# Optimization experiments

Hardware: AMD Instinct MI355X
Metric: run time of the kernel (lower is better)

## Reference

```python
import jax, jax.numpy as jnp
import numpy as np

NUM_BINS = 64  # num_bins_target == num_bins_source (defaults)
C_WIN = 1.0    # c_target == c_source (defaults)
EPS_LOG = 1e-12


def _normalise(x):
    # normalise_torch(x, 0.0, 1.0): global min-max rescale to [0, 1]
    x = x.astype(jnp.float32)
    return (x - x.min()) / (x.max() - x.min())


def _cubic_bspline(x):
    # Parzen cubic B-spline window (support |x| < 2)
    ax = jnp.abs(x)
    inner = (4.0 - 6.0 * ax * ax + 3.0 * ax * ax * ax) / 6.0
    outer = (2.0 - ax) ** 3 / 6.0
    return jnp.where(ax < 1.0, inner, jnp.where(ax < 2.0, outer, 0.0))


def setup_inputs() -> dict:
    key = jax.random.key(0)
    k1, k2 = jax.random.split(key)
    target = jax.random.uniform(k1, (2, 1, 96, 96, 96), dtype=jnp.float32)
    source = jax.random.uniform(k2, (2, 1, 96, 96, 96), dtype=jnp.float32)
    return {"target": target, "source": source}


def reference(target, source):
    # pre-processing: normalise to [0,1], flatten spatial dims -> (B, 1, N)
    t = _normalise(target).reshape(target.shape[0], target.shape[1], -1)
    s = _normalise(source).reshape(source.shape[0], source.shape[1], -1)

    # histogram bins (after normalisation max-min == 1)
    bw_t = (t.max() - t.min()) / NUM_BINS
    bw_s = (s.max() - s.min()) / NUM_BINS
    bins_t = jnp.arange(NUM_BINS, dtype=jnp.float32)[:, None] * bw_t  # (bins, 1)
    bins_s = jnp.arange(NUM_BINS, dtype=jnp.float32)[:, None] * bw_s
    eps_t = C_WIN * bw_t
    eps_s = C_WIN * bw_s

    # broadcast: (bins,1) - (B,1,N) -> (B, bins, N)
    W_t = _cubic_bspline((bins_t - t) / eps_t)
    W_s = _cubic_bspline((bins_s - s) / eps_s)

    # joint histogram: (B, bins_t, bins_s)
    hist_joint = jnp.einsum('bin,bjn->bij', W_t, W_s) / (eps_t * eps_s)

    # distributions (normalised over the WHOLE tensor, incl. batch, as in torch)
    p_joint = hist_joint / hist_joint.sum()
    p_t = p_joint.sum(axis=2)  # (B, bins_t)
    p_s = p_joint.sum(axis=1)  # (B, bins_s)

    # entropies per batch element
    H_t = -jnp.sum(p_t * jnp.log(p_t + EPS_LOG), axis=1)
    H_s = -jnp.sum(p_s * jnp.log(p_s + EPS_LOG), axis=1)
    H_j = -jnp.sum(p_joint * jnp.log(p_joint + EPS_LOG), axis=(1, 2))

    # NMI loss (nmi=True default)
    return -jnp.mean((H_t + H_s) / H_j)
```

## Files before the change

kernel.cpp:

```cpp
#include <hip/hip_runtime.h>
#include <math.h>

#define NBINS 64
#define BATCH_N 884736
#define NTOT   1769472
#define ROWB  80
#define TILE_B 5440
#define WAVE_B 10880
#define MROW 66
#define QS 190.0f
#define GBLK 216
#define GWAVES 864
#define KBLK 512

#define OFF_GHIST 256
#define OFF_KBLK 36864

typedef int  v4i __attribute__((ext_vector_type(4)));

__device__ __forceinline__ unsigned fkey(float x){
    unsigned u = __float_as_uint(x);
    return (u & 0x80000000u) ? ~u : (u | 0x80000000u);
}
__device__ __forceinline__ float fdecode(unsigned k){
    return __uint_as_float((k & 0x80000000u) ? (k ^ 0x80000000u) : ~k);
}

__device__ __forceinline__ void bw4(float u, float w[4]){
    float um = 1.f - u;
    float u2 = u*u, um2 = um*um;
    w[0] = um2*um*(1.f/6.f);
    w[3] = u2*u*(1.f/6.f);
    w[1] = 0.6666666666666667f - u2 + 0.5f*u2*u;
    w[2] = 0.6666666666666667f - um2 + 0.5f*um2*um;
}

__global__ void __launch_bounds__(256)
k_minmax(const float4* __restrict__ t4, const float4* __restrict__ s4,
         int n4, uint4* __restrict__ kblk, float* __restrict__ ghist){
    __shared__ unsigned red[4][4];

    if (blockIdx.x < 8)
        ghist[blockIdx.x*1024 + threadIdx.x] = 0.f,
        ghist[blockIdx.x*1024 + 256 + threadIdx.x] = 0.f,
        ghist[blockIdx.x*1024 + 512 + threadIdx.x] = 0.f,
        ghist[blockIdx.x*1024 + 768 + threadIdx.x] = 0.f;

    unsigned mt=0u, mnt=0u, ms=0u, mns=0u;
    int stride = gridDim.x * blockDim.x;
    for (int i = blockIdx.x*blockDim.x + threadIdx.x; i < n4; i += stride){
        float4 a = t4[i];
        float4 b = s4[i];
        mt  = max(mt,  max(max(fkey(a.x),  fkey(a.y)),  max(fkey(a.z),  fkey(a.w))));
        mnt = max(mnt, max(max(fkey(-a.x), fkey(-a.y)), max(fkey(-a.z), fkey(-a.w))));
        ms  = max(ms,  max(max(fkey(b.x),  fkey(b.y)),  max(fkey(b.z),  fkey(b.w))));
        mns = max(mns, max(max(fkey(-b.x), fkey(-b.y)), max(fkey(-b.z), fkey(-b.w))));
    }
    #pragma unroll
    for (int off = 32; off; off >>= 1){
        mt  = max(mt,  __shfl_down(mt,  off));
        mnt = max(mnt, __shfl_down(mnt, off));
        ms  = max(ms,  __shfl_down(ms,  off));
        mns = max(mns, __shfl_down(mns, off));
    }
    int wid = threadIdx.x >> 6;
    if ((threadIdx.x & 63) == 0){
        red[wid][0] = mt; red[wid][1] = mnt; red[wid][2] = ms; red[wid][3] = mns;
    }
    __syncthreads();
    if (threadIdx.x == 0){
        uint4 q;
        q.x = max(max(red[0][0], red[1][0]), max(red[2][0], red[3][0]));
        q.y = max(max(red[0][1], red[1][1]), max(red[2][1], red[3][1]));
        q.z = max(max(red[0][2], red[1][2]), max(red[2][2], red[3][2]));
        q.w = max(max(red[0][3], red[1][3]), max(red[2][3], red[3][3]));
        kblk[blockIdx.x] = q;
    }
}

__global__ void __launch_bounds__(256)
k_gemm(const float* __restrict__ t, const float* __restrict__ s,
       const uint4* __restrict__ kblk, float* __restrict__ ghist){
    __shared__ int4 smem4[2720];
    __shared__ unsigned kred[4][4];

    int tid = threadIdx.x;
    int lane = tid & 63;
    int warp = tid >> 6;
    int rrow = lane & 15;
    int kgrp = lane >> 4;
    int b = blockIdx.y;

    char* As = (char*)smem4 + warp*WAVE_B;
    char* Bs = As + TILE_B;

    {
        int4* wz = (int4*)As;
        int4 z4 = {0,0,0,0};
        #pragma unroll
        for (int i = 0; i < 11; ++i){
            int idx = i*64 + lane;
            if (idx < WAVE_B/16) wz[idx] = z4;
        }
    }

    {
        unsigned m0=0u, m1=0u, m2=0u, m3=0u;
        #pragma unroll
        for (int i = 0; i < 2; ++i){
            uint4 q = kblk[tid + i*256];
            m0 = max(m0, q.x); m1 = max(m1, q.y);
            m2 = max(m2, q.z); m3 = max(m3, q.w);
        }
        #pragma unroll
        for (int off = 32; off; off >>= 1){
            m0 = max(m0, __shfl_down(m0, off));
            m1 = max(m1, __shfl_down(m1, off));
            m2 = max(m2, __shfl_down(m2, off));
            m3 = max(m3, __shfl_down(m3, off));
        }
        if (lane == 0){
            kred[warp][0] = m0; kred[warp][1] = m1;
            kred[warp][2] = m2; kred[warp][3] = m3;
        }
        __syncthreads();
    }
    float tmax =  fdecode(max(max(kred[0][0], kred[1][0]), max(kred[2][0], kred[3][0])));
    float tmin = -fdecode(max(max(kred[0][1], kred[1][1]), max(kred[2][1], kred[3][1])));
    float smax =  fdecode(max(max(kred[0][2], kred[1][2]), max(kred[2][2], kred[3][2])));
    float smin = -fdecode(max(max(kred[0][3], kred[1][3]), max(kred[2][3], kred[3][3])));
    float tsc = 64.f / (tmax - tmin);
    float ssc = 64.f / (smax - smin);

    const float* tb = t + (size_t)b*BATCH_N;
    const float* sb = s + (size_t)b*BATCH_N;

    v4i acc[4][4];
    #pragma unroll
    for (int i = 0; i < 4; ++i)
        #pragma unroll
        for (int j = 0; j < 4; ++j)
            acc[i][j] = (v4i){0,0,0,0};

    int c0 = blockIdx.x*4 + warp;
    float tq0 = tb[(size_t)c0*64 + lane];
    float sq0 = sb[(size_t)c0*64 + lane];
    float tq1 = tb[(size_t)(c0 + GWAVES)*64 + lane];
    float sq1 = sb[(size_t)(c0 + GWAVES)*64 + lane];

    #pragma unroll 2
    for (int it = 0; it < 16; ++it){
        int cpre = c0 + (it < 14 ? (it + 2)*GWAVES : 0);
        float tnn = tb[(size_t)cpre*64 + lane];
        float snn = sb[(size_t)cpre*64 + lane];

        float vt = (tq0 - tmin) * tsc;
        float vs = (sq0 - smin) * ssc;
        int it0 = (int)floorf(vt);
        int is0 = (int)floorf(vs);
        float wt[4], wsv[4];
        bw4(vt - (float)it0, wt);
        bw4(vs - (float)is0, wsv);

        char* pa = As + it0*ROWB + lane;
        char* pb = Bs + is0*ROWB + lane;
        #pragma unroll
        for (int k = 0; k < 4; ++k){
            pa[k*ROWB] = (char)__float2int_rn(wt[k]  * QS);
            pb[k*ROWB] = (char)__float2int_rn(wsv[k] * QS);
        }

        v4i af[4], bf[4];
        #pragma unroll
        for (int m = 0; m < 4; ++m)
            af[m] = *(const v4i*)(As + (m*16 + rrow + 1)*ROWB + kgrp*16);
        #pragma unroll
        for (int n = 0; n < 4; ++n)
            bf[n] = *(const v4i*)(Bs + (n*16 + rrow + 1)*ROWB + kgrp*16);
        #pragma unroll
        for (int m = 0; m < 4; ++m)
            #pragma unroll
            for (int n = 0; n < 4; ++n)
                acc[m][n] = __builtin_amdgcn_mfma_i32_16x16x64_i8(af[m], bf[n], acc[m][n], 0, 0, 0);

        __asm__ volatile("" ::: "memory");
        #pragma unroll
        for (int k = 0; k < 4; ++k){
            pa[k*ROWB] = 0;
            pb[k*ROWB] = 0;
        }

        tq0 = tq1; sq0 = sq1;
        tq1 = tnn; sq1 = snn;
    }

    const float dq = 1.f / (QS*QS);
    float* fmw = (float*)((char*)smem4 + (warp >> 1)*(2*WAVE_B));
    __syncthreads();
    if ((warp & 1) == 0){
        #pragma unroll
        for (int m = 0; m < 4; ++m)
            #pragma unroll
            for (int n = 0; n < 4; ++n)
                #pragma unroll
                for (int r = 0; r < 4; ++r)
                    fmw[(m*16 + kgrp*4 + r)*MROW + n*16 + rrow] = (float)acc[m][n][r] * dq;
    }
    __syncthreads();
    if ((warp & 1) == 1){
        #pragma unroll
        for (int m = 0; m < 4; ++m)
            #pragma unroll
            for (int n = 0; n < 4; ++n)
                #pragma unroll
                for (int r = 0; r < 4; ++r)
                    fmw[(m*16 + kgrp*4 + r)*MROW + n*16 + rrow] += (float)acc[m][n][r] * dq;
    }
    __syncthreads();
    {
        const float* fm0 = (const float*)smem4;
        const float* fm1 = (const float*)((char*)smem4 + 2*WAVE_B);
        float* g = ghist + b*4096;
        #pragma unroll
        for (int i = 0; i < 16; ++i){
            int idx = i*256 + tid;
            int l = (idx >> 6)*MROW + (idx & 63);
            unsafeAtomicAdd(&g[idx], fm0[l] + fm1[l]);
        }
    }
}

__device__ __forceinline__ float blockReduceSum(float v, float* red){
    #pragma unroll
    for (int off = 32; off; off >>= 1) v += __shfl_down(v, off);
    int wid = threadIdx.x >> 6, lane = threadIdx.x & 63;
    __syncthreads();
    if (lane == 0) red[wid] = v;
    __syncthreads();
    return red[0] + red[1] + red[2] + red[3];
}

__global__ void k_final(const float* __restrict__ hist, float* __restrict__ out){
    __shared__ float sh[2*4096];
    __shared__ float red[4];
    int tid = threadIdx.x;
    for (int i = tid; i < 8192; i += 256) sh[i] = hist[i];
    __syncthreads();

    float loc = 0.f;
    for (int i = tid; i < 8192; i += 256) loc += sh[i];
    float total = blockReduceSum(loc, red);
    float inv = 1.f / total;

    float nmi[2];
    for (int b = 0; b < 2; ++b){
        const float* h = sh + b*4096;
        float lj = 0.f;
        for (int i = tid; i < 4096; i += 256){
            float p = h[i]*inv;
            lj += p*logf(p + 1e-12f);
        }
        float Hj = -blockReduceSum(lj, red);
        float lt = 0.f;
        if (tid < 64){
            float r = 0.f;
            for (int j = 0; j < 64; ++j) r += h[tid*64 + j];
            float p = r*inv;
            lt = p*logf(p + 1e-12f);
        }
        float Ht = -blockReduceSum(lt, red);
        float ls = 0.f;
        if (tid < 64){
            float c = 0.f;
            for (int j = 0; j < 64; ++j) c += h[j*64 + tid];
            float p = c*inv;
            ls = p*logf(p + 1e-12f);
        }
        float Hs = -blockReduceSum(ls, red);
        nmi[b] = (Ht + Hs) / Hj;
    }
    if (tid == 0) out[0] = -0.5f*(nmi[0] + nmi[1]);
}

extern "C" void kernel_launch(void* const* d_in, const int* in_sizes, int n_in,
                              void* d_out, int out_size, void* d_ws, size_t ws_size,
                              hipStream_t stream) {
    const float* t = (const float*)d_in[0];
    const float* s = (const float*)d_in[1];
    float* out = (float*)d_out;
    float* ghist = (float*)((char*)d_ws + OFF_GHIST);
    uint4* kblk  = (uint4*)((char*)d_ws + OFF_KBLK);

    k_minmax<<<KBLK, 256, 0, stream>>>((const float4*)t, (const float4*)s, NTOT/4, kblk, ghist);
    k_gemm<<<dim3(GBLK, 2), 256, 0, stream>>>(t, s, kblk, ghist);
    k_final<<<1, 256, 0, stream>>>(ghist, out);
}
```

Baseline: 97.62 us.

## Use transposed LDS reads with packed 4-byte weight scatter for int8 MFMA histogram

```diff
diff --git a/kernel.cpp b/kernel.cpp
--- a/kernel.cpp
+++ b/kernel.cpp
@@ -1,22 +1,24 @@
 #include <hip/hip_runtime.h>
 #include <math.h>
 
-#define NBINS 64
 #define BATCH_N 884736
 #define NTOT   1769472
-#define ROWB  80
-#define TILE_B 5440
-#define WAVE_B 10880
+#define NCHUNKW 18
+#define GBLK 384
+#define GWAVES 768
+#define KBLK 512
+#define QS 190.0f
+
+#define BBLK_B 1024
+#define TILE_B 6144
+#define WAVE_B 12288
 #define MROW 66
-#define QS 190.0f
-#define GBLK 216
-#define GWAVES 864
-#define KBLK 512
 
 #define OFF_GHIST 256
 #define OFF_KBLK 36864
 
-typedef int  v4i __attribute__((ext_vector_type(4)));
+typedef int v4i __attribute__((ext_vector_type(4)));
+typedef int v2i __attribute__((ext_vector_type(2)));
 
 __device__ __forceinline__ unsigned fkey(float x){
     unsigned u = __float_as_uint(x);
@@ -40,11 +42,12 @@
          int n4, uint4* __restrict__ kblk, float* __restrict__ ghist){
     __shared__ unsigned red[4][4];
 
-    if (blockIdx.x < 8)
-        ghist[blockIdx.x*1024 + threadIdx.x] = 0.f,
-        ghist[blockIdx.x*1024 + 256 + threadIdx.x] = 0.f,
-        ghist[blockIdx.x*1024 + 512 + threadIdx.x] = 0.f,
+    if (blockIdx.x < 8){
+        ghist[blockIdx.x*1024 + threadIdx.x] = 0.f;
+        ghist[blockIdx.x*1024 + 256 + threadIdx.x] = 0.f;
+        ghist[blockIdx.x*1024 + 512 + threadIdx.x] = 0.f;
         ghist[blockIdx.x*1024 + 768 + threadIdx.x] = 0.f;
+    }
 
     unsigned mt=0u, mnt=0u, ms=0u, mns=0u;
     int stride = gridDim.x * blockDim.x;
@@ -78,11 +81,11 @@
     }
 }
 
-__global__ void __launch_bounds__(256)
+__global__ void __launch_bounds__(128, 3)
 k_gemm(const float* __restrict__ t, const float* __restrict__ s,
        const uint4* __restrict__ kblk, float* __restrict__ ghist){
-    __shared__ int4 smem4[2720];
-    __shared__ unsigned kred[4][4];
+    __shared__ __align__(1024) int4 smem4[2*WAVE_B/16];
+    __shared__ unsigned kred[2][4];
 
     int tid = threadIdx.x;
     int lane = tid & 63;
@@ -98,17 +101,15 @@
         int4* wz = (int4*)As;
         int4 z4 = {0,0,0,0};
         #pragma unroll
-        for (int i = 0; i < 11; ++i){
-            int idx = i*64 + lane;
-            if (idx < WAVE_B/16) wz[idx] = z4;
-        }
+        for (int i = 0; i < 12; ++i)
+            wz[i*64 + lane] = z4;
     }
 
     {
         unsigned m0=0u, m1=0u, m2=0u, m3=0u;
         #pragma unroll
-        for (int i = 0; i < 2; ++i){
-            uint4 q = kblk[tid + i*256];
+        for (int i = 0; i < 4; ++i){
+            uint4 q = kblk[tid + i*128];
             m0 = max(m0, q.x); m1 = max(m1, q.y);
             m2 = max(m2, q.z); m3 = max(m3, q.w);
         }
@@ -125,10 +126,10 @@
         }
         __syncthreads();
     }
-    float tmax =  fdecode(max(max(kred[0][0], kred[1][0]), max(kred[2][0], kred[3][0])));
-    float tmin = -fdecode(max(max(kred[0][1], kred[1][1]), max(kred[2][1], kred[3][1])));
-    float smax =  fdecode(max(max(kred[0][2], kred[1][2]), max(kred[2][2], kred[3][2])));
-    float smin = -fdecode(max(max(kred[0][3], kred[1][3]), max(kred[2][3], kred[3][3])));
+    float tmax =  fdecode(max(kred[0][0], kred[1][0]));
+    float tmin = -fdecode(max(kred[0][1], kred[1][1]));
+    float smax =  fdecode(max(kred[0][2], kred[1][2]));
+    float smin = -fdecode(max(kred[0][3], kred[1][3]));
     float tsc = 64.f / (tmax - tmin);
     float ssc = 64.f / (smax - smin);
 
@@ -142,41 +143,90 @@
         for (int j = 0; j < 4; ++j)
             acc[i][j] = (v4i){0,0,0,0};
 
-    int c0 = blockIdx.x*4 + warp;
+    int c0 = blockIdx.x*2 + warp;
+    int vrow = ((lane >> 3) << 7) + ((lane & 7) << 4);
+    unsigned abase = (unsigned)(unsigned long long)As;
+    unsigned bbase = (unsigned)(unsigned long long)Bs;
+
     float tq0 = tb[(size_t)c0*64 + lane];
     float sq0 = sb[(size_t)c0*64 + lane];
     float tq1 = tb[(size_t)(c0 + GWAVES)*64 + lane];
     float sq1 = sb[(size_t)(c0 + GWAVES)*64 + lane];
 
-    #pragma unroll 2
-    for (int it = 0; it < 16; ++it){
-        int cpre = c0 + (it < 14 ? (it + 2)*GWAVES : 0);
+    for (int it = 0; it < NCHUNKW; ++it){
+        int cpre = c0 + (it < NCHUNKW-2 ? (it + 2)*GWAVES : 0);
         float tnn = tb[(size_t)cpre*64 + lane];
         float snn = sb[(size_t)cpre*64 + lane];
 
         float vt = (tq0 - tmin) * tsc;
+        int it0 = (int)vt;
+        float wt[4]; bw4(vt - (float)it0, wt);
+        unsigned Wa = (unsigned)__float2int_rn(wt[0]*QS)
+                    | ((unsigned)__float2int_rn(wt[1]*QS) << 8)
+                    | ((unsigned)__float2int_rn(wt[2]*QS) << 16)
+                    | ((unsigned)__float2int_rn(wt[3]*QS) << 24);
+        int ca = it0 + 15;
+        int ga = ca >> 4, sha = (ca & 15) << 3;
+        unsigned long long Wa64 = Wa;
+        unsigned long long alo = (sha < 64) ? (Wa64 << sha) : 0ull;
+        unsigned long long ahi = (sha < 64) ? (sha ? (Wa64 >> (64 - sha)) : 0ull)
+                                            : (Wa64 << (sha - 64));
+        unsigned long long asp = (sha > 96) ? (Wa64 >> (128 - sha)) : 0ull;
+
         float vs = (sq0 - smin) * ssc;
-        int it0 = (int)floorf(vt);
-        int is0 = (int)floorf(vs);
-        float wt[4], wsv[4];
-        bw4(vt - (float)it0, wt);
-        bw4(vs - (float)is0, wsv);
-
-        char* pa = As + it0*ROWB + lane;
-        char* pb = Bs + is0*ROWB + lane;
-        #pragma unroll
-        for (int k = 0; k < 4; ++k){
-            pa[k*ROWB] = (char)__float2int_rn(wt[k]  * QS);
-            pb[k*ROWB] = (char)__float2int_rn(wsv[k] * QS);
-        }
+        int is0 = (int)vs;
+        float wsv[4]; bw4(vs - (float)is0, wsv);
+        unsigned Wb = (unsigned)__float2int_rn(wsv[0]*QS)
+                    | ((unsigned)__float2int_rn(wsv[1]*QS) << 8)
+                    | ((unsigned)__float2int_rn(wsv[2]*QS) << 16)
+                    | ((unsigned)__float2int_rn(wsv[3]*QS) << 24);
+        int cb = is0 + 15;
+        int gb = cb >> 4, shb = (cb & 15) << 3;
+        unsigned long long Wb64 = Wb;
+        unsigned long long blo = (shb < 64) ? (Wb64 << shb) : 0ull;
+        unsigned long long bhi = (shb < 64) ? (shb ? (Wb64 >> (64 - shb)) : 0ull)
+                                            : (Wb64 << (shb - 64));
+        unsigned long long bsp = (shb > 96) ? (Wb64 >> (128 - shb)) : 0ull;
+
+        char* pa = As + ga*BBLK_B + vrow;
+        char* pb = Bs + gb*BBLK_B + vrow;
+        *(v4i*)pa            = (v4i){(int)alo, (int)(alo>>32), (int)ahi, (int)(ahi>>32)};
+        *(v4i*)(pa + BBLK_B) = (v4i){(int)asp, (int)(asp>>32), 0, 0};
+        *(v4i*)pb            = (v4i){(int)blo, (int)(blo>>32), (int)bhi, (int)(bhi>>32)};
+        *(v4i*)(pb + BBLK_B) = (v4i){(int)bsp, (int)(bsp>>32), 0, 0};
+
+        __asm__ volatile("" ::: "memory");
+
+        v2i a00,a01,a10,a11,a20,a21,a30,a31;
+        v2i b00,b01,b10,b11,b20,b21,b30,b31;
+        asm volatile("ds_read_b64_tr_b8 %0, %1 offset:1024" : "=v"(a00) : "v"(abase));
+        asm volatile("ds_read_b64_tr_b8 %0, %1 offset:1536" : "=v"(a01) : "v"(abase));
+        asm volatile("ds_read_b64_tr_b8 %0, %1 offset:2048" : "=v"(a10) : "v"(abase));
+        asm volatile("ds_read_b64_tr_b8 %0, %1 offset:2560" : "=v"(a11) : "v"(abase));
+        asm volatile("ds_read_b64_tr_b8 %0, %1 offset:3072" : "=v"(a20) : "v"(abase));
+        asm volatile("ds_read_b64_tr_b8 %0, %1 offset:3584" : "=v"(a21) : "v"(abase));
+        asm volatile("ds_read_b64_tr_b8 %0, %1 offset:4096" : "=v"(a30) : "v"(abase));
+        asm volatile("ds_read_b64_tr_b8 %0, %1 offset:4608" : "=v"(a31) : "v"(abase));
+        asm volatile("ds_read_b64_tr_b8 %0, %1 offset:1024" : "=v"(b00) : "v"(bbase));
+        asm volatile("ds_read_b64_tr_b8 %0, %1 offset:1536" : "=v"(b01) : "v"(bbase));
+        asm volatile("ds_read_b64_tr_b8 %0, %1 offset:2048" : "=v"(b10) : "v"(bbase));
+        asm volatile("ds_read_b64_tr_b8 %0, %1 offset:2560" : "=v"(b11) : "v"(bbase));
+        asm volatile("ds_read_b64_tr_b8 %0, %1 offset:3072" : "=v"(b20) : "v"(bbase));
+        asm volatile("ds_read_b64_tr_b8 %0, %1 offset:3584" : "=v"(b21) : "v"(bbase));
+        asm volatile("ds_read_b64_tr_b8 %0, %1 offset:4096" : "=v"(b30) : "v"(bbase));
+        asm volatile("ds_read_b64_tr_b8 %0, %1 offset:4608" : "=v"(b31) : "v"(bbase));
+        asm volatile("s_waitcnt lgkmcnt(0)" ::: "memory");
+        __builtin_amdgcn_sched_barrier(0);
 
         v4i af[4], bf[4];
-        #pragma unroll
-        for (int m = 0; m < 4; ++m)
-            af[m] = *(const v4i*)(As + (m*16 + rrow + 1)*ROWB + kgrp*16);
-        #pragma unroll
-        for (int n = 0; n < 4; ++n)
-            bf[n] = *(const v4i*)(Bs + (n*16 + rrow + 1)*ROWB + kgrp*16);
+        af[0] = (v4i){a00.x, a00.y, a01.x, a01.y};
+        af[1] = (v4i){a10.x, a10.y, a11.x, a11.y};
+        af[2] = (v4i){a20.x, a20.y, a21.x, a21.y};
+        af[3] = (v4i){a30.x, a30.y, a31.x, a31.y};
+        bf[0] = (v4i){b00.x, b00.y, b01.x, b01.y};
+        bf[1] = (v4i){b10.x, b10.y, b11.x, b11.y};
+        bf[2] = (v4i){b20.x, b20.y, b21.x, b21.y};
+        bf[3] = (v4i){b30.x, b30.y, b31.x, b31.y};
         #pragma unroll
         for (int m = 0; m < 4; ++m)
             #pragma unroll
@@ -184,10 +234,10 @@
                 acc[m][n] = __builtin_amdgcn_mfma_i32_16x16x64_i8(af[m], bf[n], acc[m][n], 0, 0, 0);
 
         __asm__ volatile("" ::: "memory");
-        #pragma unroll
-        for (int k = 0; k < 4; ++k){
-            pa[k*ROWB] = 0;
-            pb[k*ROWB] = 0;
+        {
+            v4i z = (v4i){0,0,0,0};
+            *(v4i*)pa = z; *(v4i*)(pa + BBLK_B) = z;
+            *(v4i*)pb = z; *(v4i*)(pb + BBLK_B) = z;
         }
 
         tq0 = tq1; sq0 = sq1;
@@ -195,37 +245,34 @@
     }
 
     const float dq = 1.f / (QS*QS);
-    float* fmw = (float*)((char*)smem4 + (warp >> 1)*(2*WAVE_B));
-    __syncthreads();
-    if ((warp & 1) == 0){
+    float* fm = (float*)smem4;
+    __syncthreads();
+    if (warp == 0){
         #pragma unroll
         for (int m = 0; m < 4; ++m)
             #pragma unroll
             for (int n = 0; n < 4; ++n)
                 #pragma unroll
                 for (int r = 0; r < 4; ++r)
-                    fmw[(m*16 + kgrp*4 + r)*MROW + n*16 + rrow] = (float)acc[m][n][r] * dq;
-    }
-    __syncthreads();
-    if ((warp & 1) == 1){
+                    fm[(m*16 + kgrp*4 + r)*MROW + n*16 + rrow] = (float)acc[m][n][r] * dq;
+    }
+    __syncthreads();
+    if (warp == 1){
         #pragma unroll
         for (int m = 0; m < 4; ++m)
             #pragma unroll
             for (int n = 0; n < 4; ++n)
                 #pragma unroll
                 for (int r = 0; r < 4; ++r)
-                    fmw[(m*16 + kgrp*4 + r)*MROW + n*16 + rrow] += (float)acc[m][n][r] * dq;
+                    fm[(m*16 + kgrp*4 + r)*MROW + n*16 + rrow] += (float)acc[m][n][r] * dq;
     }
     __syncthreads();
     {
-        const float* fm0 = (const float*)smem4;
-        const float* fm1 = (const float*)((char*)smem4 + 2*WAVE_B);
         float* g = ghist + b*4096;
         #pragma unroll
-        for (int i = 0; i < 16; ++i){
-            int idx = i*256 + tid;
-            int l = (idx >> 6)*MROW + (idx & 63);
-            unsafeAtomicAdd(&g[idx], fm0[l] + fm1[l]);
+        for (int i = 0; i < 32; ++i){
+            int idx = i*128 + tid;
+            unsafeAtomicAdd(&g[idx], fm[(idx >> 6)*MROW + (idx & 63)]);
         }
     }
 }
@@ -292,6 +339,6 @@
     uint4* kblk  = (uint4*)((char*)d_ws + OFF_KBLK);
 
     k_minmax<<<KBLK, 256, 0, stream>>>((const float4*)t, (const float4*)s, NTOT/4, kblk, ghist);
-    k_gemm<<<dim3(GBLK, 2), 256, 0, stream>>>(t, s, kblk, ghist);
+    k_gemm<<<dim3(GBLK, 2), 128, 0, stream>>>(t, s, kblk, ghist);
     k_final<<<1, 256, 0, stream>>>(ghist, out);
 }
```

New measurement: 107.1 us. +9.7%, slower.

## Fuse min-max, histogram GEMM and entropy into one cooperative kernel

Applied to the files above, without the earlier changes.

```diff
diff --git a/kernel.cpp b/kernel.cpp
--- a/kernel.cpp
+++ b/kernel.cpp
@@ -1,22 +1,28 @@
 #include <hip/hip_runtime.h>
+#include <hip/hip_cooperative_groups.h>
 #include <math.h>
 
-#define NBINS 64
+namespace cg = cooperative_groups;
+
 #define BATCH_N 884736
 #define NTOT   1769472
-#define ROWB  80
+#define GBX 128
+#define NBLK 256
+#define WPB 12
+#define THREADS 768
+#define GWAVES 1536
+#define NCHUNK 9
+#define MM4 1728
+#define ROWB 80
 #define TILE_B 5440
 #define WAVE_B 10880
 #define MROW 66
 #define QS 190.0f
-#define GBLK 216
-#define GWAVES 864
-#define KBLK 512
 
 #define OFF_GHIST 256
 #define OFF_KBLK 36864
 
-typedef int  v4i __attribute__((ext_vector_type(4)));
+typedef int v4i __attribute__((ext_vector_type(4)));
 
 __device__ __forceinline__ unsigned fkey(float x){
     unsigned u = __float_as_uint(x);
@@ -35,82 +41,89 @@
     w[2] = 0.6666666666666667f - um2 + 0.5f*um2*um;
 }
 
-__global__ void __launch_bounds__(256)
-k_minmax(const float4* __restrict__ t4, const float4* __restrict__ s4,
-         int n4, uint4* __restrict__ kblk, float* __restrict__ ghist){
-    __shared__ unsigned red[4][4];
-
-    if (blockIdx.x < 8)
-        ghist[blockIdx.x*1024 + threadIdx.x] = 0.f,
-        ghist[blockIdx.x*1024 + 256 + threadIdx.x] = 0.f,
-        ghist[blockIdx.x*1024 + 512 + threadIdx.x] = 0.f,
-        ghist[blockIdx.x*1024 + 768 + threadIdx.x] = 0.f;
-
-    unsigned mt=0u, mnt=0u, ms=0u, mns=0u;
-    int stride = gridDim.x * blockDim.x;
-    for (int i = blockIdx.x*blockDim.x + threadIdx.x; i < n4; i += stride){
-        float4 a = t4[i];
-        float4 b = s4[i];
-        mt  = max(mt,  max(max(fkey(a.x),  fkey(a.y)),  max(fkey(a.z),  fkey(a.w))));
-        mnt = max(mnt, max(max(fkey(-a.x), fkey(-a.y)), max(fkey(-a.z), fkey(-a.w))));
-        ms  = max(ms,  max(max(fkey(b.x),  fkey(b.y)),  max(fkey(b.z),  fkey(b.w))));
-        mns = max(mns, max(max(fkey(-b.x), fkey(-b.y)), max(fkey(-b.z), fkey(-b.w))));
-    }
+__device__ __forceinline__ float bsum(float v, float* red){
     #pragma unroll
-    for (int off = 32; off; off >>= 1){
-        mt  = max(mt,  __shfl_down(mt,  off));
-        mnt = max(mnt, __shfl_down(mnt, off));
-        ms  = max(ms,  __shfl_down(ms,  off));
-        mns = max(mns, __shfl_down(mns, off));
-    }
-    int wid = threadIdx.x >> 6;
-    if ((threadIdx.x & 63) == 0){
-        red[wid][0] = mt; red[wid][1] = mnt; red[wid][2] = ms; red[wid][3] = mns;
-    }
-    __syncthreads();
-    if (threadIdx.x == 0){
-        uint4 q;
-        q.x = max(max(red[0][0], red[1][0]), max(red[2][0], red[3][0]));
-        q.y = max(max(red[0][1], red[1][1]), max(red[2][1], red[3][1]));
-        q.z = max(max(red[0][2], red[1][2]), max(red[2][2], red[3][2]));
-        q.w = max(max(red[0][3], red[1][3]), max(red[2][3], red[3][3]));
-        kblk[blockIdx.x] = q;
-    }
-}
-
-__global__ void __launch_bounds__(256)
-k_gemm(const float* __restrict__ t, const float* __restrict__ s,
-       const uint4* __restrict__ kblk, float* __restrict__ ghist){
-    __shared__ int4 smem4[2720];
-    __shared__ unsigned kred[4][4];
+    for (int off = 32; off; off >>= 1) v += __shfl_down(v, off);
+    int wid = threadIdx.x >> 6, lane = threadIdx.x & 63;
+    __syncthreads();
+    if (lane == 0) red[wid] = v;
+    __syncthreads();
+    float s = 0.f;
+    #pragma unroll
+    for (int j = 0; j < WPB; ++j) s += red[j];
+    return s;
+}
+
+__global__ void __launch_bounds__(THREADS, 3)
+k_nmi(const float* __restrict__ t, const float* __restrict__ s,
+      float* __restrict__ ghist, unsigned* __restrict__ kblk,
+      float* __restrict__ out){
+    __shared__ int4 smem4[WPB*WAVE_B/16];
+    __shared__ unsigned kred[WPB][4];
+    __shared__ float redf[WPB];
+
+    cg::grid_group grid = cg::this_grid();
 
     int tid = threadIdx.x;
     int lane = tid & 63;
     int warp = tid >> 6;
     int rrow = lane & 15;
     int kgrp = lane >> 4;
-    int b = blockIdx.y;
-
-    char* As = (char*)smem4 + warp*WAVE_B;
-    char* Bs = As + TILE_B;
-
+    int bx = blockIdx.x, by = blockIdx.y;
+    int linear = by*GBX + bx;
+
+    if (linear < 8){
+        for (int i = tid; i < 1024; i += THREADS)
+            __hip_atomic_store(&ghist[linear*1024 + i], 0.f,
+                               __ATOMIC_RELAXED, __HIP_MEMORY_SCOPE_AGENT);
+    }
     {
-        int4* wz = (int4*)As;
-        int4 z4 = {0,0,0,0};
-        #pragma unroll
-        for (int i = 0; i < 11; ++i){
-            int idx = i*64 + lane;
-            if (idx < WAVE_B/16) wz[idx] = z4;
-        }
-    }
+        const float4* t4 = (const float4*)t;
+        const float4* s4 = (const float4*)s;
+        unsigned mt=0u, mnt=0u, ms=0u, mns=0u;
+        int i0 = linear*MM4;
+        for (int i = i0 + tid; i < i0 + MM4; i += THREADS){
+            float4 a = t4[i];
+            float4 b = s4[i];
+            mt  = max(mt,  max(max(fkey(a.x),  fkey(a.y)),  max(fkey(a.z),  fkey(a.w))));
+            mnt = max(mnt, max(max(fkey(-a.x), fkey(-a.y)), max(fkey(-a.z), fkey(-a.w))));
+            ms  = max(ms,  max(max(fkey(b.x),  fkey(b.y)),  max(fkey(b.z),  fkey(b.w))));
+            mns = max(mns, max(max(fkey(-b.x), fkey(-b.y)), max(fkey(-b.z), fkey(-b.w))));
+        }
+        #pragma unroll
+        for (int off = 32; off; off >>= 1){
+            mt  = max(mt,  __shfl_down(mt,  off));
+            mnt = max(mnt, __shfl_down(mnt, off));
+            ms  = max(ms,  __shfl_down(ms,  off));
+            mns = max(mns, __shfl_down(mns, off));
+        }
+        if (lane == 0){
+            kred[warp][0] = mt; kred[warp][1] = mnt;
+            kred[warp][2] = ms; kred[warp][3] = mns;
+        }
+        __syncthreads();
+        if (tid == 0){
+            unsigned q0=0u,q1=0u,q2=0u,q3=0u;
+            #pragma unroll
+            for (int j = 0; j < WPB; ++j){
+                q0 = max(q0, kred[j][0]); q1 = max(q1, kred[j][1]);
+                q2 = max(q2, kred[j][2]); q3 = max(q3, kred[j][3]);
+            }
+            __hip_atomic_store(&kblk[linear*4+0], q0, __ATOMIC_RELAXED, __HIP_MEMORY_SCOPE_AGENT);
+            __hip_atomic_store(&kblk[linear*4+1], q1, __ATOMIC_RELAXED, __HIP_MEMORY_SCOPE_AGENT);
+            __hip_atomic_store(&kblk[linear*4+2], q2, __ATOMIC_RELAXED, __HIP_MEMORY_SCOPE_AGENT);
+            __hip_atomic_store(&kblk[linear*4+3], q3, __ATOMIC_RELAXED, __HIP_MEMORY_SCOPE_AGENT);
+        }
+    }
+    grid.sync();
 
     {
         unsigned m0=0u, m1=0u, m2=0u, m3=0u;
-        #pragma unroll
-        for (int i = 0; i < 2; ++i){
-            uint4 q = kblk[tid + i*256];
-            m0 = max(m0, q.x); m1 = max(m1, q.y);
-            m2 = max(m2, q.z); m3 = max(m3, q.w);
+        if (tid < NBLK){
+            m0 = __hip_atomic_load(&kblk[tid*4+0], __ATOMIC_RELAXED, __HIP_MEMORY_SCOPE_AGENT);
+            m1 = __hip_atomic_load(&kblk[tid*4+1], __ATOMIC_RELAXED, __HIP_MEMORY_SCOPE_AGENT);
+            m2 = __hip_atomic_load(&kblk[tid*4+2], __ATOMIC_RELAXED, __HIP_MEMORY_SCOPE_AGENT);
+            m3 = __hip_atomic_load(&kblk[tid*4+3], __ATOMIC_RELAXED, __HIP_MEMORY_SCOPE_AGENT);
         }
         #pragma unroll
         for (int off = 32; off; off >>= 1){
@@ -125,15 +138,32 @@
         }
         __syncthreads();
     }
-    float tmax =  fdecode(max(max(kred[0][0], kred[1][0]), max(kred[2][0], kred[3][0])));
-    float tmin = -fdecode(max(max(kred[0][1], kred[1][1]), max(kred[2][1], kred[3][1])));
-    float smax =  fdecode(max(max(kred[0][2], kred[1][2]), max(kred[2][2], kred[3][2])));
-    float smin = -fdecode(max(max(kred[0][3], kred[1][3]), max(kred[2][3], kred[3][3])));
+    unsigned k0=0u,k1=0u,k2=0u,k3=0u;
+    #pragma unroll
+    for (int j = 0; j < WPB; ++j){
+        k0 = max(k0, kred[j][0]); k1 = max(k1, kred[j][1]);
+        k2 = max(k2, kred[j][2]); k3 = max(k3, kred[j][3]);
+    }
+    float tmax =  fdecode(k0), tmin = -fdecode(k1);
+    float smax =  fdecode(k2), smin = -fdecode(k3);
     float tsc = 64.f / (tmax - tmin);
     float ssc = 64.f / (smax - smin);
 
-    const float* tb = t + (size_t)b*BATCH_N;
-    const float* sb = s + (size_t)b*BATCH_N;
+    char* As = (char*)smem4 + warp*WAVE_B;
+    char* Bs = As + TILE_B;
+
+    {
+        int4* wz = (int4*)As;
+        int4 z4 = {0,0,0,0};
+        #pragma unroll
+        for (int i = 0; i < 11; ++i){
+            int idx = i*64 + lane;
+            if (idx < WAVE_B/16) wz[idx] = z4;
+        }
+    }
+
+    const float* tb = t + (size_t)by*BATCH_N;
+    const float* sb = s + (size_t)by*BATCH_N;
 
     v4i acc[4][4];
     #pragma unroll
@@ -142,15 +172,14 @@
         for (int j = 0; j < 4; ++j)
             acc[i][j] = (v4i){0,0,0,0};
 
-    int c0 = blockIdx.x*4 + warp;
+    int c0 = bx*WPB + warp;
     float tq0 = tb[(size_t)c0*64 + lane];
     float sq0 = sb[(size_t)c0*64 + lane];
     float tq1 = tb[(size_t)(c0 + GWAVES)*64 + lane];
     float sq1 = sb[(size_t)(c0 + GWAVES)*64 + lane];
 
-    #pragma unroll 2
-    for (int it = 0; it < 16; ++it){
-        int cpre = c0 + (it < 14 ? (it + 2)*GWAVES : 0);
+    for (int it = 0; it < NCHUNK; ++it){
+        int cpre = c0 + (it < NCHUNK-2 ? (it + 2)*GWAVES : 0);
         float tnn = tb[(size_t)cpre*64 + lane];
         float snn = sb[(size_t)cpre*64 + lane];
 
@@ -218,49 +247,38 @@
     }
     __syncthreads();
     {
-        const float* fm0 = (const float*)smem4;
-        const float* fm1 = (const float*)((char*)smem4 + 2*WAVE_B);
-        float* g = ghist + b*4096;
-        #pragma unroll
-        for (int i = 0; i < 16; ++i){
-            int idx = i*256 + tid;
+        float* g = ghist + by*4096;
+        for (int idx = tid; idx < 4096; idx += THREADS){
             int l = (idx >> 6)*MROW + (idx & 63);
-            unsafeAtomicAdd(&g[idx], fm0[l] + fm1[l]);
-        }
-    }
-}
-
-__device__ __forceinline__ float blockReduceSum(float v, float* red){
-    #pragma unroll
-    for (int off = 32; off; off >>= 1) v += __shfl_down(v, off);
-    int wid = threadIdx.x >> 6, lane = threadIdx.x & 63;
-    __syncthreads();
-    if (lane == 0) red[wid] = v;
-    __syncthreads();
-    return red[0] + red[1] + red[2] + red[3];
-}
-
-__global__ void k_final(const float* __restrict__ hist, float* __restrict__ out){
-    __shared__ float sh[2*4096];
-    __shared__ float red[4];
-    int tid = threadIdx.x;
-    for (int i = tid; i < 8192; i += 256) sh[i] = hist[i];
+            float v = 0.f;
+            #pragma unroll
+            for (int p = 0; p < 6; ++p)
+                v += *((const float*)((const char*)smem4 + p*(2*WAVE_B)) + l);
+            unsafeAtomicAdd(&g[idx], v);
+        }
+    }
+    grid.sync();
+
+    if (linear != 0) return;
+    float* sh = (float*)smem4;
+    for (int i = tid; i < 8192; i += THREADS)
+        sh[i] = __hip_atomic_load(&ghist[i], __ATOMIC_RELAXED, __HIP_MEMORY_SCOPE_AGENT);
     __syncthreads();
 
     float loc = 0.f;
-    for (int i = tid; i < 8192; i += 256) loc += sh[i];
-    float total = blockReduceSum(loc, red);
+    for (int i = tid; i < 8192; i += THREADS) loc += sh[i];
+    float total = bsum(loc, redf);
     float inv = 1.f / total;
 
     float nmi[2];
     for (int b = 0; b < 2; ++b){
         const float* h = sh + b*4096;
         float lj = 0.f;
-        for (int i = tid; i < 4096; i += 256){
+        for (int i = tid; i < 4096; i += THREADS){
             float p = h[i]*inv;
             lj += p*logf(p + 1e-12f);
         }
-        float Hj = -blockReduceSum(lj, red);
+        float Hj = -bsum(lj, redf);
         float lt = 0.f;
         if (tid < 64){
             float r = 0.f;
@@ -268,7 +286,7 @@
             float p = r*inv;
             lt = p*logf(p + 1e-12f);
         }
-        float Ht = -blockReduceSum(lt, red);
+        float Ht = -bsum(lt, redf);
         float ls = 0.f;
         if (tid < 64){
             float c = 0.f;
@@ -276,7 +294,7 @@
             float p = c*inv;
             ls = p*logf(p + 1e-12f);
         }
-        float Hs = -blockReduceSum(ls, red);
+        float Hs = -bsum(ls, redf);
         nmi[b] = (Ht + Hs) / Hj;
     }
     if (tid == 0) out[0] = -0.5f*(nmi[0] + nmi[1]);
@@ -287,11 +305,11 @@
                               hipStream_t stream) {
     const float* t = (const float*)d_in[0];
     const float* s = (const float*)d_in[1];
-    float* out = (float*)d_out;
+    float* outp = (float*)d_out;
     float* ghist = (float*)((char*)d_ws + OFF_GHIST);
-    uint4* kblk  = (uint4*)((char*)d_ws + OFF_KBLK);
-
-    k_minmax<<<KBLK, 256, 0, stream>>>((const float4*)t, (const float4*)s, NTOT/4, kblk, ghist);
-    k_gemm<<<dim3(GBLK, 2), 256, 0, stream>>>(t, s, kblk, ghist);
-    k_final<<<1, 256, 0, stream>>>(ghist, out);
-}
+    unsigned* kblk = (unsigned*)((char*)d_ws + OFF_KBLK);
+
+    void* args[] = {(void*)&t, (void*)&s, (void*)&ghist, (void*)&kblk, (void*)&outp};
+    hipLaunchCooperativeKernel((void*)k_nmi, dim3(GBX, 2), dim3(THREADS),
+                               args, 0, stream);
+}
```

Measured after the change: 144.4 us. 47.9% more time.
